# Optimization experiments

Measured on AMD Instinct MI355X. Metric: run time of the kernel, lower is better.

## Reference

```python
import jax, jax.numpy as jnp
import numpy as np

NUM_TOKENS = 16384
INPUT_DIM = 4096
NUM_EXPERTS = 64
TOPK = 2


def setup_inputs() -> dict:
    key = jax.random.key(0)
    k1, k2 = jax.random.split(key)
    tokens = jax.random.normal(k1, (NUM_TOKENS, INPUT_DIM), dtype=jnp.float32)
    # nn.Linear(input_dim, num_experts).weight has shape [num_experts, input_dim]
    W = jax.random.normal(k2, (NUM_EXPERTS, INPUT_DIM), dtype=jnp.float32) * (1.0 / np.sqrt(INPUT_DIM))
    return {"tokens": tokens, "W": W}


def reference(tokens, W):
    # logits: [num_tokens, num_experts] = tokens @ W.T
    logits = jnp.einsum("td,ed->te", tokens, W)
    scores = jax.nn.softmax(logits, axis=-1)
    topk_scores, topk_indices = jax.lax.top_k(scores, TOPK)
    return topk_scores, topk_indices
```

## Files before the change

kernel.cpp:

```cpp
#include <hip/hip_runtime.h>
#include <math.h>

#define NTOK 16384
#define DIM  4096
#define NEXP 64
#define KS   2
#define KSL  (DIM / KS)
#define BK   64
#define NCH  (KSL / BK)
#define BM   64

typedef __fp16 f16x8  __attribute__((ext_vector_type(8)));
typedef __fp16 f16x2  __attribute__((ext_vector_type(2)));
typedef float  f32x16 __attribute__((ext_vector_type(16)));

__device__ __forceinline__ void gl_lds16(const void* g, void* l) {
  __builtin_amdgcn_global_load_lds(
      (const __attribute__((address_space(1))) void*)g,
      (__attribute__((address_space(3))) void*)l, 16, 0, 0);
}

__global__ __launch_bounds__(256) void split_w(
    const float* __restrict__ W,
    __fp16* __restrict__ Wh,
    __fp16* __restrict__ Wl)
{
  const int i = blockIdx.x * 256 + threadIdx.x;
  const float w = W[i];
  const __fp16 h = (__fp16)w;
  const float r = w - (float)h;
  Wh[i] = h;
  Wl[i] = (__fp16)r;
}

__global__ __launch_bounds__(256, 2) void router_mfma(
    const float* __restrict__ tokens,
    const __fp16* __restrict__ Wh,
    const __fp16* __restrict__ Wl,
    float* __restrict__ partial)
{
  __shared__ float  As[2][BM * BK];
  __shared__ __fp16 Bh[2][NEXP * BK];
  __shared__ __fp16 Bl[2][NEXP * BK];

  const int tid  = threadIdx.x;
  const int wid  = tid >> 6;
  const int lane = tid & 63;
  const int rc2  = lane & 31;
  const int q2   = lane >> 5;
  const int wr   = wid >> 1;
  const int ec   = wid & 1;
  const int s    = blockIdx.x & (KS - 1);
  const int tb   = (blockIdx.x >> 1) * BM;
  const int kbase = s * KSL;

  const int l16 = lane >> 4;
  const int aj  = lane & 15;
  const float* ap0 = tokens + (size_t)(tb + 16*wid +  0 + l16) * DIM + kbase + ((aj ^ ( 0 + l16)) << 2);
  const float* ap1 = tokens + (size_t)(tb + 16*wid +  4 + l16) * DIM + kbase + ((aj ^ ( 4 + l16)) << 2);
  const float* ap2 = tokens + (size_t)(tb + 16*wid +  8 + l16) * DIM + kbase + ((aj ^ ( 8 + l16)) << 2);
  const float* ap3 = tokens + (size_t)(tb + 16*wid + 12 + l16) * DIM + kbase + ((aj ^ (12 + l16)) << 2);
  const int l8 = lane >> 3;
  const int bj = lane & 7;
  const size_t bo0 = (size_t)(16*wid + 0 + l8) * DIM + kbase + ((bj ^ l8) << 3);
  const size_t bo1 = (size_t)(16*wid + 8 + l8) * DIM + kbase + ((bj ^ l8) << 3);
  const __fp16* bh0s = Wh + bo0; const __fp16* bh1s = Wh + bo1;
  const __fp16* bl0s = Wl + bo0; const __fp16* bl1s = Wl + bo1;

#define STAGE(buf, c) {                                          \
    const int ko = (c) * BK;                                     \
    gl_lds16(ap0 + ko, &As[buf][(16 * wid +  0) * BK]);          \
    gl_lds16(ap1 + ko, &As[buf][(16 * wid +  4) * BK]);          \
    gl_lds16(ap2 + ko, &As[buf][(16 * wid +  8) * BK]);          \
    gl_lds16(ap3 + ko, &As[buf][(16 * wid + 12) * BK]);          \
    gl_lds16(bh0s + ko, &Bh[buf][(16 * wid + 0) * BK]);          \
    gl_lds16(bh1s + ko, &Bh[buf][(16 * wid + 8) * BK]);          \
    gl_lds16(bl0s + ko, &Bl[buf][(16 * wid + 0) * BK]);          \
    gl_lds16(bl1s + ko, &Bl[buf][(16 * wid + 8) * BK]);          \
  }

  f32x16 acc = {0,0,0,0, 0,0,0,0, 0,0,0,0, 0,0,0,0};

  const int akey = rc2 & 15;
  const int bkey = rc2 & 7;
  const int Arow = (32 * wr + rc2) * BK;
  const int Brow = (32 * ec + rc2) * BK;

#define KSTEP(buf, kk) {                                                     \
    const int u0 = 4 * (kk) + 2 * q2;                                        \
    const float4 a0 = *(const float4*)(&As[buf][Arow + ((u0    ) ^ akey) * 4]); \
    const float4 a1 = *(const float4*)(&As[buf][Arow + ((u0 + 1) ^ akey) * 4]); \
    const int ub = ((2 * (kk) + q2) ^ bkey) * 8;                             \
    const f16x8 bhv = *(const f16x8*)(&Bh[buf][Brow + ub]);                  \
    const f16x8 blv = *(const f16x8*)(&Bl[buf][Brow + ub]);                  \
    const f16x2 h0 = __builtin_amdgcn_cvt_pkrtz(a0.x, a0.y);                 \
    const f16x2 h1 = __builtin_amdgcn_cvt_pkrtz(a0.z, a0.w);                 \
    const f16x2 h2 = __builtin_amdgcn_cvt_pkrtz(a1.x, a1.y);                 \
    const f16x2 h3 = __builtin_amdgcn_cvt_pkrtz(a1.z, a1.w);                 \
    const f16x2 m0 = __builtin_amdgcn_cvt_pkrtz(a0.x - (float)h0[0],         \
                                                a0.y - (float)h0[1]);        \
    const f16x2 m1 = __builtin_amdgcn_cvt_pkrtz(a0.z - (float)h1[0],         \
                                                a0.w - (float)h1[1]);        \
    const f16x2 m2 = __builtin_amdgcn_cvt_pkrtz(a1.x - (float)h2[0],         \
                                                a1.y - (float)h2[1]);        \
    const f16x2 m3 = __builtin_amdgcn_cvt_pkrtz(a1.z - (float)h3[0],         \
                                                a1.w - (float)h3[1]);        \
    const f16x8 Ah = {h0[0],h0[1],h1[0],h1[1],h2[0],h2[1],h3[0],h3[1]};      \
    const f16x8 Am = {m0[0],m0[1],m1[0],m1[1],m2[0],m2[1],m3[0],m3[1]};      \
    acc = __builtin_amdgcn_mfma_f32_32x32x16_f16(Ah, bhv, acc, 0, 0, 0);     \
    acc = __builtin_amdgcn_mfma_f32_32x32x16_f16(Ah, blv, acc, 0, 0, 0);     \
    acc = __builtin_amdgcn_mfma_f32_32x32x16_f16(Am, bhv, acc, 0, 0, 0);     \
  }

#define COMP(buf) { KSTEP(buf, 0); KSTEP(buf, 1); KSTEP(buf, 2); KSTEP(buf, 3); }

  STAGE(0, 0);
  __syncthreads();

  for (int c = 0; c < NCH; c += 2) {
    if (c + 1 < NCH) STAGE(1, c + 1);
    COMP(0);
    __syncthreads();
    if (c + 2 < NCH) STAGE(0, c + 2);
    COMP(1);
    __syncthreads();
  }
#undef STAGE
#undef COMP
#undef KSTEP

  float* P = partial + ((size_t)s * NTOK + tb + 32 * wr) * NEXP + 32 * ec;
  #pragma unroll
  for (int reg = 0; reg < 16; ++reg) {
    const int row = (reg & 3) + 8 * (reg >> 2) + 4 * q2;
    P[(size_t)row * NEXP + rc2] = acc[reg];
  }
}

__global__ __launch_bounds__(64) void router_finish(
    const float* __restrict__ partial,
    float* __restrict__ out)
{
  const int t = blockIdx.x * 64 + threadIdx.x;

  float l[NEXP];
  const float* p0 = partial + (size_t)t * NEXP;
  #pragma unroll
  for (int qq = 0; qq < 16; ++qq) {
    const float4 v = *(const float4*)(p0 + qq * 4);
    l[qq*4+0] = v.x; l[qq*4+1] = v.y; l[qq*4+2] = v.z; l[qq*4+3] = v.w;
  }
  #pragma unroll
  for (int s = 1; s < KS; ++s) {
    const float* p = partial + ((size_t)s * NTOK + t) * NEXP;
    #pragma unroll
    for (int qq = 0; qq < 16; ++qq) {
      const float4 v = *(const float4*)(p + qq * 4);
      l[qq*4+0] += v.x; l[qq*4+1] += v.y; l[qq*4+2] += v.z; l[qq*4+3] += v.w;
    }
  }

  float t1v = l[0]; int t1i = 0;
  float t2v = -INFINITY; int t2i = NEXP;
  #pragma unroll
  for (int e = 1; e < NEXP; ++e) {
    const float v = l[e];
    if (v > t1v) { t2v = t1v; t2i = t1i; t1v = v; t1i = e; }
    else if (v > t2v) { t2v = v; t2i = e; }
  }

  float ssum = 0.f;
  #pragma unroll
  for (int e = 0; e < NEXP; ++e) ssum += expf(l[e] - t1v);

  const float inv = 1.0f / ssum;
  out[t * 2 + 0] = inv;
  out[t * 2 + 1] = expf(t2v - t1v) * inv;
  out[2 * NTOK + t * 2 + 0] = (float)t1i;
  out[2 * NTOK + t * 2 + 1] = (float)t2i;
}

extern "C" void kernel_launch(void* const* d_in, const int* in_sizes, int n_in,
                              void* d_out, int out_size, void* d_ws, size_t ws_size,
                              hipStream_t stream) {
  const float* tokens = (const float*)d_in[0];
  const float* W      = (const float*)d_in[1];
  float* out          = (float*)d_out;

  __fp16* Wh = (__fp16*)d_ws;
  __fp16* Wl = Wh + (size_t)NEXP * DIM;
  float* partial = (float*)((char*)d_ws + (size_t)2 * NEXP * DIM * sizeof(__fp16));

  split_w<<<(NEXP * DIM) / 256, 256, 0, stream>>>(W, Wh, Wl);
  router_mfma<<<(NTOK / BM) * KS, 256, 0, stream>>>(tokens, Wh, Wl, partial);
  router_finish<<<NTOK / 64, 64, 0, stream>>>(partial, out);
}
```

Measured before the change: 72.56 us.

## Triple-buffer LDS pipeline with vmcnt waits, split K four ways, halve BK

Splits K across four blocks instead of two and halves the K-chunk to 32. It replaces the double-buffered __syncthreads loop with a three-stage ring that uses explicit s_waitcnt vmcnt and raw barriers, so two chunk loads stay in flight while one is computed. Occupancy hint rises to 3 blocks per CU. The goal is more memory-level parallelism and more blocks to hide load latency, at the cost of doubling partial-sum writes and reads in the finish kernel and relying on a hand-counted vmcnt that assumes exact load counts.

```diff
diff --git a/kernel.cpp b/kernel.cpp
--- a/kernel.cpp
+++ b/kernel.cpp
@@ -4,9 +4,9 @@
 #define NTOK 16384
 #define DIM  4096
 #define NEXP 64
-#define KS   2
+#define KS   4
 #define KSL  (DIM / KS)
-#define BK   64
+#define BK   32
 #define NCH  (KSL / BK)
 #define BM   64
 
@@ -33,15 +33,15 @@
   Wl[i] = (__fp16)r;
 }
 
-__global__ __launch_bounds__(256, 2) void router_mfma(
+__global__ __launch_bounds__(256, 3) void router_mfma(
     const float* __restrict__ tokens,
     const __fp16* __restrict__ Wh,
     const __fp16* __restrict__ Wl,
     float* __restrict__ partial)
 {
-  __shared__ float  As[2][BM * BK];
-  __shared__ __fp16 Bh[2][NEXP * BK];
-  __shared__ __fp16 Bl[2][NEXP * BK];
+  __shared__ float  As[3][BM * BK];
+  __shared__ __fp16 Bh[3][NEXP * BK];
+  __shared__ __fp16 Bl[3][NEXP * BK];
 
   const int tid  = threadIdx.x;
   const int wid  = tid >> 6;
@@ -51,40 +51,33 @@
   const int wr   = wid >> 1;
   const int ec   = wid & 1;
   const int s    = blockIdx.x & (KS - 1);
-  const int tb   = (blockIdx.x >> 1) * BM;
+  const int tb   = (blockIdx.x >> 2) * BM;
   const int kbase = s * KSL;
 
-  const int l16 = lane >> 4;
-  const int aj  = lane & 15;
-  const float* ap0 = tokens + (size_t)(tb + 16*wid +  0 + l16) * DIM + kbase + ((aj ^ ( 0 + l16)) << 2);
-  const float* ap1 = tokens + (size_t)(tb + 16*wid +  4 + l16) * DIM + kbase + ((aj ^ ( 4 + l16)) << 2);
-  const float* ap2 = tokens + (size_t)(tb + 16*wid +  8 + l16) * DIM + kbase + ((aj ^ ( 8 + l16)) << 2);
-  const float* ap3 = tokens + (size_t)(tb + 16*wid + 12 + l16) * DIM + kbase + ((aj ^ (12 + l16)) << 2);
-  const int l8 = lane >> 3;
-  const int bj = lane & 7;
-  const size_t bo0 = (size_t)(16*wid + 0 + l8) * DIM + kbase + ((bj ^ l8) << 3);
-  const size_t bo1 = (size_t)(16*wid + 8 + l8) * DIM + kbase + ((bj ^ l8) << 3);
-  const __fp16* bh0s = Wh + bo0; const __fp16* bh1s = Wh + bo1;
-  const __fp16* bl0s = Wl + bo0; const __fp16* bl1s = Wl + bo1;
+  const int a_tl = lane >> 3, a_j = lane & 7;
+  const float* asrc0 = tokens + (size_t)(tb + 16 * wid + a_tl) * DIM + kbase
+                       + ((a_j ^ a_tl) << 2);
+  const float* asrc1 = asrc0 + (size_t)8 * DIM;
+  const int b_el = lane >> 2, b_j = lane & 3;
+  const size_t boff = (size_t)(16 * wid + b_el) * DIM + kbase
+                      + ((b_j ^ (b_el & 3)) << 3);
+  const __fp16* bsrc_h = Wh + boff;
+  const __fp16* bsrc_l = Wl + boff;
 
-#define STAGE(buf, c) {                                          \
-    const int ko = (c) * BK;                                     \
-    gl_lds16(ap0 + ko, &As[buf][(16 * wid +  0) * BK]);          \
-    gl_lds16(ap1 + ko, &As[buf][(16 * wid +  4) * BK]);          \
-    gl_lds16(ap2 + ko, &As[buf][(16 * wid +  8) * BK]);          \
-    gl_lds16(ap3 + ko, &As[buf][(16 * wid + 12) * BK]);          \
-    gl_lds16(bh0s + ko, &Bh[buf][(16 * wid + 0) * BK]);          \
-    gl_lds16(bh1s + ko, &Bh[buf][(16 * wid + 8) * BK]);          \
-    gl_lds16(bl0s + ko, &Bl[buf][(16 * wid + 0) * BK]);          \
-    gl_lds16(bl1s + ko, &Bl[buf][(16 * wid + 8) * BK]);          \
+#define STAGE(buf, c) {                                  \
+    const int ko = (c) * BK;                             \
+    gl_lds16(asrc0 + ko, &As[buf][(16 * wid) * 32]);     \
+    gl_lds16(asrc1 + ko, &As[buf][(16 * wid + 8) * 32]); \
+    gl_lds16(bsrc_h + ko, &Bh[buf][(16 * wid) * 32]);    \
+    gl_lds16(bsrc_l + ko, &Bl[buf][(16 * wid) * 32]);    \
   }
 
   f32x16 acc = {0,0,0,0, 0,0,0,0, 0,0,0,0, 0,0,0,0};
 
-  const int akey = rc2 & 15;
-  const int bkey = rc2 & 7;
-  const int Arow = (32 * wr + rc2) * BK;
-  const int Brow = (32 * ec + rc2) * BK;
+  const int akey = rc2 & 7;
+  const int bkey = rc2 & 3;
+  const int Arow = (32 * wr + rc2) * 32;
+  const int Brow = (32 * ec + rc2) * 32;
 
 #define KSTEP(buf, kk) {                                                     \
     const int u0 = 4 * (kk) + 2 * q2;                                        \
@@ -112,22 +105,28 @@
     acc = __builtin_amdgcn_mfma_f32_32x32x16_f16(Am, bhv, acc, 0, 0, 0);     \
   }
 
-#define COMP(buf) { KSTEP(buf, 0); KSTEP(buf, 1); KSTEP(buf, 2); KSTEP(buf, 3); }
+#define COMP(buf) { KSTEP(buf, 0); KSTEP(buf, 1); }
+
+#define VM(n) asm volatile("s_waitcnt vmcnt(" #n ")" ::: "memory")
+#define BAR() __builtin_amdgcn_s_barrier()
 
   STAGE(0, 0);
-  __syncthreads();
+  STAGE(1, 1);
 
-  for (int c = 0; c < NCH; c += 2) {
-    if (c + 1 < NCH) STAGE(1, c + 1);
-    COMP(0);
-    __syncthreads();
-    if (c + 2 < NCH) STAGE(0, c + 2);
-    COMP(1);
-    __syncthreads();
+  for (int i = 0; i < 10; ++i) {
+    const int c = 3 * i;
+    VM(4); BAR(); STAGE(2, c + 2); COMP(0);
+    VM(4); BAR(); STAGE(0, c + 3); COMP(1);
+    VM(4); BAR(); STAGE(1, c + 4); COMP(2);
   }
+  VM(4); BAR(); COMP(0);
+  VM(0); BAR(); COMP(1);
+
 #undef STAGE
 #undef COMP
 #undef KSTEP
+#undef VM
+#undef BAR
 
   float* P = partial + ((size_t)s * NTOK + tb + 32 * wr) * NEXP + 32 * ec;
   #pragma unroll
```

Measured after the change: 106.1 us. 1.46x slower.
